# Kernel optimization log

Measured on AMD Instinct MI355X. Metric: run time of the kernel, lower is better.

Reference implementation:

```python
import jax, jax.numpy as jnp
import numpy as np

NS, NC, T, NB = 32, 16, 64, 512
NSC = NS + NC


def setup_inputs() -> dict:
    key = jax.random.key(0)
    k1, k2, k3, k4, k5 = jax.random.split(key, 5)
    # SPD cost matrices so Quu is invertible (as assumed by the LQR math)
    L = jax.random.normal(k1, (NB, T, NSC, NSC), jnp.float32) * 0.1
    Q = L @ jnp.swapaxes(L, -1, -2) + jnp.eye(NSC, dtype=jnp.float32)
    p = jax.random.normal(k2, (NB, T, NSC), jnp.float32)
    x_init = jax.random.normal(k3, (NB, NS), jnp.float32)
    # stable-ish LTI dynamics
    A = 0.9 * jnp.eye(NS, dtype=jnp.float32) + 0.01 * jax.random.normal(k4, (NS, NS), jnp.float32)
    B = 0.1 * jax.random.normal(k5, (NS, NC), jnp.float32)
    dt = jnp.float32(0.1)
    return {"x_init": x_init, "Q": Q, "p": p, "A": A, "B": B, "dt": dt}


def _lqr(x_init, Q, p, A, B):
    ns, nc = A.shape[0], B.shape[1]
    nb, Th = Q.shape[0], Q.shape[1]
    dtype = Q.dtype

    # --- nominal rollout with zero control: x_{t+1} = A x_t ---
    def roll(x, _):
        return x @ A.T, x
    _, cx = jax.lax.scan(roll, x_init, None, length=Th)   # [T,B,ns] states x_0..x_{T-1}
    cu = jnp.zeros((Th, nb, nc), dtype)                    # current_u = 0
    xu = jnp.concatenate([cx, cu], -1)                     # [T,B,nsc]

    Qs = jnp.swapaxes(Q, 0, 1)                             # [T,B,nsc,nsc]
    ps = jnp.swapaxes(p, 0, 1)                             # [T,B,nsc]
    p_new = jnp.einsum('tbij,tbj->tbi', Qs, xu) + ps       # [T,B,nsc]

    F = jnp.concatenate([A, B], axis=1)                    # [ns, nsc]

    # --- backward Riccati recursion (V=v=0 at t=T-1 makes Qt=Q[T-1]) ---
    def bwd(carry, inp):
        V, v = carry                                       # [B,ns,ns], [B,ns]
        Qt_in, qt_in = inp
        Qt = Qt_in + jnp.einsum('si,bst,tj->bij', F, V, F)
        qt = qt_in + v @ F                                 # F^T v
        Qxx, Qxu = Qt[:, :ns, :ns], Qt[:, :ns, ns:]
        Qux, Quu = Qt[:, ns:, :ns], Qt[:, ns:, ns:]
        qx, qu = qt[:, :ns], qt[:, ns:]
        Quu_inv = jnp.linalg.pinv(Quu)
        Kt = -Quu_inv @ Qux                                # [B,nc,ns]
        kt = -jnp.einsum('bij,bj->bi', Quu_inv, qu)        # [B,nc]
        KtT = jnp.swapaxes(Kt, -1, -2)
        Vn = Qxx + Qxu @ Kt + KtT @ Qux + KtT @ Quu @ Kt
        vn = (qx + jnp.einsum('bij,bj->bi', Qxu, kt)
              + jnp.einsum('bij,bj->bi', KtT, qu)
              + jnp.einsum('bij,bj->bi', KtT @ Quu, kt))
        return (Vn, vn), (Kt, kt)

    V0 = jnp.zeros((nb, ns, ns), dtype)
    v0 = jnp.zeros((nb, ns), dtype)
    _, (Ks, ks) = jax.lax.scan(bwd, (V0, v0), (Qs, p_new), reverse=True)

    # --- forward rollout with feedback policy ---
    def fwd(carry, inp):
        xt, cost = carry
        Kt, kt, cxt, cut, Qt, pt = inp
        dut = jnp.einsum('bij,bj->bi', Kt, xt - cxt) + kt
        ut = dut + cut
        xut = jnp.concatenate([xt, ut], -1)
        cost = cost + 0.5 * jnp.einsum('bi,bij,bj->b', xut, Qt, xut) + (xut * pt).sum(-1)
        xn = xt @ A.T + ut @ B.T
        return (xn, cost), (xt, ut)

    (_, cost), (xs, us) = jax.lax.scan(
        fwd, (x_init, jnp.zeros(nb, dtype)), (Ks, ks, cx, cu, Qs, ps))
    x = jnp.swapaxes(xs, 0, 1)   # [B,T,ns]  (states x_0..x_{T-1}, matching x[...,:-1,:])
    u = jnp.swapaxes(us, 0, 1)   # [B,T,nc]
    return x, u, cost


def reference(x_init, Q, p, A, B, dt):
    # dt only matters for nonlinear relinearization; with constant LTI (A,B) it is unused.
    return _lqr(x_init, Q, p, A, B)
```

## Files before the change

kernel.cpp:

```cpp
#include <hip/hip_runtime.h>


#define NSd 32
#define NCd 16
#define Td 64
#define NBd 512
#define NSCd 48

typedef __bf16 bf16x8 __attribute__((ext_vector_type(8)));
typedef __bf16 bf16x4 __attribute__((ext_vector_type(4)));
typedef float f32x4 __attribute__((ext_vector_type(4)));

#define MFMA16(a, b, c) __builtin_amdgcn_mfma_f32_16x16x32_bf16(a, b, c, 0, 0, 0)

#define XOFF ((size_t)0)
#define UOFF ((size_t)NBd * Td * NSd)
#define COFF (UOFF + (size_t)NBd * Td * NCd)

__device__ __forceinline__ float rdl(float v, int l) {
  return __uint_as_float(__builtin_amdgcn_readlane(__float_as_uint(v), l));
}

union LdsU {
  struct {
    __bf16 FTh[48][32], FTl[48][32];
    __bf16 Vh[32][32], Vl[32][32];
    __bf16 WTh[48][32], WTl[48][32];
    __bf16 Xh[32][32], Xl[32][32];
    __bf16 KTh[32][32], KTl[32][32];
    float Quu[16][17];
    float qt[48];
    float vv[32];
    float kt[16];
  } bw;
  struct {
    float K2T[2][16 * 36];
    float kv2[2][16];
    float d[32];
    float xs[32];
    float uu[16];
  } fw;
};

__global__ __launch_bounds__(256, 2) void lqr_kernel(
    const float* __restrict__ x_init, const float* __restrict__ Qg,
    const float* __restrict__ pg, const float* __restrict__ Ag,
    const float* __restrict__ Bg, float* __restrict__ out,
    float* __restrict__ wsK, float* __restrict__ wskv) {
  const int b = blockIdx.x;
  const int tid = threadIdx.x;
  const int w = tid >> 6;
  const int lane = tid & 63;
  const int fn = lane & 15;
  const int quad = lane >> 4;
  const int k0 = quad * 8;

  __shared__ __attribute__((aligned(16))) float sQ[2304];
  __shared__ float scx[Td][NSd];
  __shared__ float sFf[NSd][NSCd];
  __shared__ __attribute__((aligned(16))) LdsU U;
  __shared__ float scostp[4];

  for (int idx = tid; idx < 1536; idx += 256) {
    int i = idx / 48, j = idx - i * 48;
    sFf[i][j] = (j < 32) ? Ag[i * 32 + j] : Bg[i * 16 + (j - 32)];
  }
  for (int idx = tid; idx < 1536; idx += 256) {
    int a = idx >> 5, k = idx & 31;
    float f = (a < 32) ? Ag[k * 32 + a] : Bg[k * 16 + (a - 32)];
    __bf16 h = (__bf16)f;
    U.bw.FTh[a][k] = h;
    U.bw.FTl[a][k] = (__bf16)(f - (float)h);
  }
  for (int idx = tid; idx < 1024; idx += 256) {
    int r = idx >> 5, c = idx & 31;
    __bf16 z = (__bf16)0.f;
    U.bw.Vh[r][c] = z; U.bw.Vl[r][c] = z;
    U.bw.Xh[r][c] = z; U.bw.Xl[r][c] = z;
    U.bw.KTh[r][c] = z; U.bw.KTl[r][c] = z;
  }
  if (tid < 32) {
    scx[0][tid] = x_init[b * 32 + tid];
    U.bw.vv[tid] = 0.f;
  }
  {
    const float4* src = (const float4*)(Qg + ((size_t)b * Td + 63) * 2304);
    float4* dst = (float4*)sQ;
    dst[tid] = src[tid];
    dst[tid + 256] = src[tid + 256];
    if (tid < 64) dst[tid + 512] = src[tid + 512];
  }
  float ppf = 0.f;
  if (w == 3 && lane < 48) ppf = pg[((size_t)b * Td + 63) * 48 + lane];
  __syncthreads();

  if (w == 0) {
    for (int t2 = 0; t2 < Td - 1; ++t2) {
      if (lane < 32) {
        float acc = 0.f;
#pragma unroll
        for (int j = 0; j < 32; j += 4) {
          float4 a4 = *(const float4*)&sFf[lane][j];
          acc += a4.x * scx[t2][j] + a4.y * scx[t2][j + 1] +
                 a4.z * scx[t2][j + 2] + a4.w * scx[t2][j + 3];
        }
        scx[t2 + 1][lane] = acc;
      }
    }
  }
  __syncthreads();

  float cAcc = 0.f;
  float dAcc = 0.f;

  for (int t = Td - 1; t >= 0; --t) {
    const int sw = 3 - (t & 1);
    float4 pf0, pf1, pf2;
    float ppfn;
    if (t > 0) {
      const float4* src = (const float4*)(Qg + ((size_t)b * Td + (t - 1)) * 2304);
      pf0 = src[tid];
      pf1 = src[tid + 256];
      if (tid < 64) pf2 = src[tid + 512];
      if (w == 3 && lane < 48) ppfn = pg[((size_t)b * Td + t - 1) * 48 + lane];
    }
    if (w < 3) {
      const int I = w;
      bf16x8 aH = *(const bf16x8*)&U.bw.FTh[16 * I + fn][k0];
      bf16x8 aL = *(const bf16x8*)&U.bw.FTl[16 * I + fn][k0];
#pragma unroll
      for (int J = 0; J < 2; ++J) {
        bf16x8 bH = *(const bf16x8*)&U.bw.Vh[16 * J + fn][k0];
        bf16x8 bL = *(const bf16x8*)&U.bw.Vl[16 * J + fn][k0];
        f32x4 acc = {0.f, 0.f, 0.f, 0.f};
        acc = MFMA16(aL, bH, acc);
        acc = MFMA16(aH, bL, acc);
        acc = MFMA16(aH, bH, acc);
#pragma unroll
        for (int r = 0; r < 4; ++r) {
          float v = acc[r];
          __bf16 h = (__bf16)v;
          U.bw.WTh[16 * I + 4 * quad + r][16 * J + fn] = h;
          U.bw.WTl[16 * I + 4 * quad + r][16 * J + fn] = (__bf16)(v - (float)h);
        }
      }
    } else if (lane < 48) {
      float acc1 = ppf;
#pragma unroll
      for (int k = 0; k < 32; ++k) acc1 += sQ[k * 48 + lane] * scx[t][k];
      if (lane < 32) cAcc += 0.5f * scx[t][lane] * (acc1 + ppf);
      float acc = acc1;
#pragma unroll
      for (int k = 0; k < 32; ++k) acc += U.bw.vv[k] * sFf[k][lane];
      U.bw.qt[lane] = acc;
    }
    if (t > 0 && w == 3) ppf = ppfn;
    __syncthreads();

    f32x4 accQ = {0.f, 0.f, 0.f, 0.f};
    if (w < 2) {
      const int I = w;
      bf16x8 aH = *(const bf16x8*)&U.bw.WTh[16 * I + fn][k0];
      bf16x8 aL = *(const bf16x8*)&U.bw.WTl[16 * I + fn][k0];
      {
        bf16x8 bH = *(const bf16x8*)&U.bw.FTh[16 * I + fn][k0];
        bf16x8 bL = *(const bf16x8*)&U.bw.FTl[16 * I + fn][k0];
#pragma unroll
        for (int r = 0; r < 4; ++r)
          accQ[r] = sQ[(16 * I + 4 * quad + r) * 48 + 16 * I + fn];
        accQ = MFMA16(aL, bH, accQ);
        accQ = MFMA16(aH, bL, accQ);
        accQ = MFMA16(aH, bH, accQ);
      }
      {
        bf16x8 bH = *(const bf16x8*)&U.bw.FTh[32 + fn][k0];
        bf16x8 bL = *(const bf16x8*)&U.bw.FTl[32 + fn][k0];
        f32x4 acc;
#pragma unroll
        for (int r = 0; r < 4; ++r)
          acc[r] = sQ[(16 * I + 4 * quad + r) * 48 + 32 + fn];
        acc = MFMA16(aL, bH, acc);
        acc = MFMA16(aH, bL, acc);
        acc = MFMA16(aH, bH, acc);
#pragma unroll
        for (int r = 0; r < 4; ++r) {
          float v = acc[r];
          __bf16 h = (__bf16)v;
          U.bw.Xh[16 * I + 4 * quad + r][fn] = h;
          U.bw.Xl[16 * I + 4 * quad + r][fn] = (__bf16)(v - (float)h);
        }
      }
    } else if (w == 2) {
      bf16x8 aH = *(const bf16x8*)&U.bw.WTh[fn][k0];
      bf16x8 aL = *(const bf16x8*)&U.bw.WTl[fn][k0];
      bf16x8 bH = *(const bf16x8*)&U.bw.FTh[16 + fn][k0];
      bf16x8 bL = *(const bf16x8*)&U.bw.FTl[16 + fn][k0];
#pragma unroll
      for (int r = 0; r < 4; ++r)
        accQ[r] = sQ[(4 * quad + r) * 48 + 16 + fn];
      accQ = MFMA16(aL, bH, accQ);
      accQ = MFMA16(aH, bL, accQ);
      accQ = MFMA16(aH, bH, accQ);
    } else {
      bf16x8 aH = *(const bf16x8*)&U.bw.WTh[32 + fn][k0];
      bf16x8 aL = *(const bf16x8*)&U.bw.WTl[32 + fn][k0];
      bf16x8 bH = *(const bf16x8*)&U.bw.FTh[32 + fn][k0];
      bf16x8 bL = *(const bf16x8*)&U.bw.FTl[32 + fn][k0];
      f32x4 acc;
#pragma unroll
      for (int r = 0; r < 4; ++r)
        acc[r] = sQ[(32 + 4 * quad + r) * 48 + 32 + fn];
      acc = MFMA16(aL, bH, acc);
      acc = MFMA16(aH, bL, acc);
      acc = MFMA16(aH, bH, acc);
#pragma unroll
      for (int r = 0; r < 4; ++r) U.bw.Quu[4 * quad + r][fn] = acc[r];
    }
    __syncthreads();

    if (t > 0) {
      float4* dst = (float4*)sQ;
      dst[tid] = pf0;
      dst[tid + 256] = pf1;
      if (tid < 64) dst[tid + 512] = pf2;
    }

    if (w == sw) {
      float rhs[16];
      if (lane < 32) {
        bf16x8 xh0 = *(const bf16x8*)&U.bw.Xh[lane][0];
        bf16x8 xh1 = *(const bf16x8*)&U.bw.Xh[lane][8];
        bf16x8 xl0 = *(const bf16x8*)&U.bw.Xl[lane][0];
        bf16x8 xl1 = *(const bf16x8*)&U.bw.Xl[lane][8];
#pragma unroll
        for (int i = 0; i < 8; ++i) {
          rhs[i] = (float)xh0[i] + (float)xl0[i];
          rhs[8 + i] = (float)xh1[i] + (float)xl1[i];
        }
      } else {
#pragma unroll
        for (int i = 0; i < 16; ++i) rhs[i] = U.bw.qt[32 + i];
      }
      float quu[16];
#pragma unroll
      for (int i = 0; i < 16; ++i) quu[i] = U.bw.Quu[i][fn];
#pragma unroll
      for (int r = 0; r < 15; ++r) {
        float inv = __builtin_amdgcn_rcpf(rdl(quu[r], r));
#pragma unroll
        for (int i = r + 1; i < 16; ++i) {
          float m = rdl(quu[i], r) * inv;
          rhs[i] -= m * rhs[r];
          quu[i] -= m * quu[r];
        }
      }
      float xx[16];
#pragma unroll
      for (int r = 15; r >= 0; --r) {
        float s = rhs[r];
#pragma unroll
        for (int c = r + 1; c < 16; ++c) s -= rdl(quu[r], c) * xx[c];
        xx[r] = s * __builtin_amdgcn_rcpf(rdl(quu[r], r));
      }
      if (lane < 32) {
        bf16x8 h0, l0, h1, l1;
#pragma unroll
        for (int u = 0; u < 8; ++u) {
          float kv = -xx[u];
          __bf16 hh = (__bf16)kv;
          h0[u] = hh; l0[u] = (__bf16)(kv - (float)hh);
          float kv2 = -xx[8 + u];
          __bf16 hh2 = (__bf16)kv2;
          h1[u] = hh2; l1[u] = (__bf16)(kv2 - (float)hh2);
        }
        *(bf16x8*)&U.bw.KTh[lane][0] = h0;
        *(bf16x8*)&U.bw.KTh[lane][8] = h1;
        *(bf16x8*)&U.bw.KTl[lane][0] = l0;
        *(bf16x8*)&U.bw.KTl[lane][8] = l1;
        float4* dst = (float4*)(wsK + (((size_t)b * Td + t) * 32 + lane) * 16);
        float4 v0 = {-xx[0], -xx[1], -xx[2], -xx[3]};
        float4 v1 = {-xx[4], -xx[5], -xx[6], -xx[7]};
        float4 v2 = {-xx[8], -xx[9], -xx[10], -xx[11]};
        float4 v3 = {-xx[12], -xx[13], -xx[14], -xx[15]};
        dst[0] = v0; dst[1] = v1; dst[2] = v2; dst[3] = v3;
      } else if (lane == 32) {
#pragma unroll
        for (int u = 0; u < 16; ++u) U.bw.kt[u] = -xx[u];
        float4* dst = (float4*)(wskv + ((size_t)b * Td + t) * 16);
        float4 v0 = {-xx[0], -xx[1], -xx[2], -xx[3]};
        float4 v1 = {-xx[4], -xx[5], -xx[6], -xx[7]};
        float4 v2 = {-xx[8], -xx[9], -xx[10], -xx[11]};
        float4 v3 = {-xx[12], -xx[13], -xx[14], -xx[15]};
        dst[0] = v0; dst[1] = v1; dst[2] = v2; dst[3] = v3;
        float s = 0.f;
#pragma unroll
        for (int i = 0; i < 16; ++i) s += U.bw.qt[32 + i] * xx[i];
        dAcc -= 0.5f * s;
      }
      if (sw == 3) {
        float acc = 0.f;
        bf16x8 xh0, xh1, xl0, xl1;
        if (lane < 32) {
          xh0 = *(const bf16x8*)&U.bw.Xh[lane][0];
          xh1 = *(const bf16x8*)&U.bw.Xh[lane][8];
          xl0 = *(const bf16x8*)&U.bw.Xl[lane][0];
          xl1 = *(const bf16x8*)&U.bw.Xl[lane][8];
          acc = U.bw.qt[lane];
        }
#pragma unroll
        for (int u = 0; u < 8; ++u) {
          float kt0 = -rdl(xx[u], 32);
          float kt1 = -rdl(xx[8 + u], 32);
          if (lane < 32) {
            acc += ((float)xh0[u] + (float)xl0[u]) * kt0;
            acc += ((float)xh1[u] + (float)xl1[u]) * kt1;
          }
        }
        if (lane < 32) U.bw.vv[lane] = acc;
      }
    }
    __syncthreads();

    if (w == 0) {
      bf16x8 aH = *(const bf16x8*)&U.bw.Xh[fn][k0];
      bf16x8 aL = *(const bf16x8*)&U.bw.Xl[fn][k0];
      bf16x8 bH = *(const bf16x8*)&U.bw.KTh[fn][k0];
      bf16x8 bL = *(const bf16x8*)&U.bw.KTl[fn][k0];
      accQ = MFMA16(aL, bH, accQ);
      accQ = MFMA16(aH, bL, accQ);
      accQ = MFMA16(aH, bH, accQ);
#pragma unroll
      for (int r = 0; r < 4; ++r) {
        float v = accQ[r];
        __bf16 h = (__bf16)v;
        U.bw.Vh[4 * quad + r][fn] = h;
        U.bw.Vl[4 * quad + r][fn] = (__bf16)(v - (float)h);
      }
    } else if (w == 1) {
      bf16x8 aH = *(const bf16x8*)&U.bw.Xh[16 + fn][k0];
      bf16x8 aL = *(const bf16x8*)&U.bw.Xl[16 + fn][k0];
      bf16x8 bH = *(const bf16x8*)&U.bw.KTh[16 + fn][k0];
      bf16x8 bL = *(const bf16x8*)&U.bw.KTl[16 + fn][k0];
      accQ = MFMA16(aL, bH, accQ);
      accQ = MFMA16(aH, bL, accQ);
      accQ = MFMA16(aH, bH, accQ);
#pragma unroll
      for (int r = 0; r < 4; ++r) {
        float v = accQ[r];
        __bf16 h = (__bf16)v;
        U.bw.Vh[16 + 4 * quad + r][16 + fn] = h;
        U.bw.Vl[16 + 4 * quad + r][16 + fn] = (__bf16)(v - (float)h);
      }
    } else if (w == 2) {
      bf16x8 aH = *(const bf16x8*)&U.bw.Xh[fn][k0];
      bf16x8 aL = *(const bf16x8*)&U.bw.Xl[fn][k0];
      bf16x8 bH = *(const bf16x8*)&U.bw.KTh[16 + fn][k0];
      bf16x8 bL = *(const bf16x8*)&U.bw.KTl[16 + fn][k0];
      accQ = MFMA16(aL, bH, accQ);
      accQ = MFMA16(aH, bL, accQ);
      accQ = MFMA16(aH, bH, accQ);
      bf16x4 th, tl;
#pragma unroll
      for (int r = 0; r < 4; ++r) {
        float v = accQ[r];
        __bf16 h = (__bf16)v;
        __bf16 l = (__bf16)(v - (float)h);
        U.bw.Vh[4 * quad + r][16 + fn] = h;
        U.bw.Vl[4 * quad + r][16 + fn] = l;
        th[r] = h; tl[r] = l;
      }
      *(bf16x4*)&U.bw.Vh[16 + fn][4 * quad] = th;
      *(bf16x4*)&U.bw.Vl[16 + fn][4 * quad] = tl;
    } else if (sw == 2) {
      if (lane < 32) {
        bf16x8 xh0 = *(const bf16x8*)&U.bw.Xh[lane][0];
        bf16x8 xh1 = *(const bf16x8*)&U.bw.Xh[lane][8];
        bf16x8 xl0 = *(const bf16x8*)&U.bw.Xl[lane][0];
        bf16x8 xl1 = *(const bf16x8*)&U.bw.Xl[lane][8];
        float acc = U.bw.qt[lane];
#pragma unroll
        for (int u = 0; u < 8; ++u) {
          acc += ((float)xh0[u] + (float)xl0[u]) * U.bw.kt[u];
          acc += ((float)xh1[u] + (float)xl1[u]) * U.bw.kt[8 + u];
        }
        U.bw.vv[lane] = acc;
      }
    }
    __syncthreads();
  }

  if (w == 3) {
    float rv = (lane < 32) ? cAcc : 0.f;
    rv += __shfl_down(rv, 32);
    rv += __shfl_down(rv, 16);
    rv += __shfl_down(rv, 8);
    rv += __shfl_down(rv, 4);
    rv += __shfl_down(rv, 2);
    rv += __shfl_down(rv, 1);
    if (lane == 0) scostp[0] = rv;
  }
  if (lane == 32 && w >= 2) scostp[w - 1] = dAcc;
  __syncthreads();

  if (w == 0) {
    {
      const float4* src = (const float4*)(wsK + ((size_t)b * Td) * 512);
      float4 ka = src[lane * 2], kb = src[lane * 2 + 1];
      int jj = lane >> 1, ib = (lane & 1) * 8;
      float* kt2 = U.fw.K2T[0];
      kt2[(ib + 0) * 36 + jj] = ka.x; kt2[(ib + 1) * 36 + jj] = ka.y;
      kt2[(ib + 2) * 36 + jj] = ka.z; kt2[(ib + 3) * 36 + jj] = ka.w;
      kt2[(ib + 4) * 36 + jj] = kb.x; kt2[(ib + 5) * 36 + jj] = kb.y;
      kt2[(ib + 6) * 36 + jj] = kb.z; kt2[(ib + 7) * 36 + jj] = kb.w;
      if (lane < 16) U.fw.kv2[0][lane] = wskv[(size_t)b * Td * 16 + lane];
    }
    float xr = (lane < 32) ? scx[0][lane] : 0.f;
    for (int t = 0; t < Td; ++t) {
      const int cur = t & 1, nxt = cur ^ 1;
      float4 pa, pb;
      float pk;
      if (t < Td - 1) {
        const float4* src = (const float4*)(wsK + ((size_t)b * Td + t + 1) * 512);
        pa = src[lane * 2];
        pb = src[lane * 2 + 1];
        if (lane < 16) pk = wskv[((size_t)b * Td + t + 1) * 16 + lane];
      }
      if (lane < 32) {
        U.fw.d[lane] = xr - scx[t][lane];
        U.fw.xs[lane] = xr;
        out[XOFF + ((size_t)b * Td + t) * 32 + lane] = xr;
      }
      if (lane < 16) {
        float uv = U.fw.kv2[cur][lane];
        const float* kr = &U.fw.K2T[cur][lane * 36];
#pragma unroll
        for (int j4 = 0; j4 < 8; ++j4) {
          float4 kk = *(const float4*)&kr[j4 * 4];
          float4 dd = *(const float4*)&U.fw.d[j4 * 4];
          uv += kk.x * dd.x + kk.y * dd.y + kk.z * dd.z + kk.w * dd.w;
        }
        U.fw.uu[lane] = uv;
        out[UOFF + ((size_t)b * Td + t) * 16 + lane] = uv;
      }
      if (lane < 32) {
        float acc = 0.f;
#pragma unroll
        for (int j4 = 0; j4 < 8; ++j4) {
          float4 ff = *(const float4*)&sFf[lane][j4 * 4];
          float4 xv = *(const float4*)&U.fw.xs[j4 * 4];
          acc += ff.x * xv.x + ff.y * xv.y + ff.z * xv.z + ff.w * xv.w;
        }
#pragma unroll
        for (int j4 = 0; j4 < 4; ++j4) {
          float4 ff = *(const float4*)&sFf[lane][32 + j4 * 4];
          float4 uv = *(const float4*)&U.fw.uu[j4 * 4];
          acc += ff.x * uv.x + ff.y * uv.y + ff.z * uv.z + ff.w * uv.w;
        }
        xr = acc;
      }
      if (t < Td - 1) {
        int jj = lane >> 1, ib = (lane & 1) * 8;
        float* kt2 = U.fw.K2T[nxt];
        kt2[(ib + 0) * 36 + jj] = pa.x; kt2[(ib + 1) * 36 + jj] = pa.y;
        kt2[(ib + 2) * 36 + jj] = pa.z; kt2[(ib + 3) * 36 + jj] = pa.w;
        kt2[(ib + 4) * 36 + jj] = pb.x; kt2[(ib + 5) * 36 + jj] = pb.y;
        kt2[(ib + 6) * 36 + jj] = pb.z; kt2[(ib + 7) * 36 + jj] = pb.w;
        if (lane < 16) U.fw.kv2[nxt][lane] = pk;
      }
    }
    if (lane == 0) out[COFF + b] = scostp[0] + scostp[1] + scostp[2];
  }
}

extern "C" void kernel_launch(void* const* d_in, const int* in_sizes, int n_in,
                              void* d_out, int out_size, void* d_ws, size_t ws_size,
                              hipStream_t stream) {
  const float* x_init = (const float*)d_in[0];
  const float* Qg = (const float*)d_in[1];
  const float* pg = (const float*)d_in[2];
  const float* Ag = (const float*)d_in[3];
  const float* Bg = (const float*)d_in[4];
  float* out = (float*)d_out;
  float* wsK = (float*)d_ws;
  float* wskv = wsK + (size_t)NBd * Td * NSd * NCd;
  lqr_kernel<<<NBd, 256, 0, stream>>>(x_init, Qg, pg, Ag, Bg, out, wsK, wskv);
}
```

Baseline: 667.7 us.

## Collapse LQR block to a single wavefront, removing block barriers

Each batch block now runs as one 64-lane wavefront instead of four waves. All the Riccati MFMA work, the Quu solve and the vector updates run serially in that wave, with no __syncthreads. The union LDS layout is split into separate arrays. This removes per-step barrier latency and cross-wave handoffs, but each wave now carries all the MFMA and scalar work serially, and the Q prefetch needs 9 float4 registers per lane. In exchange, more blocks may fit per CU.

Measured after the change: 772.9 us. 1.16x slower.

```diff
diff --git a/kernel.cpp b/kernel.cpp
--- a/kernel.cpp
+++ b/kernel.cpp
@@ -5,7 +5,6 @@
 #define NCd 16
 #define Td 64
 #define NBd 512
-#define NSCd 48
 
 typedef __bf16 bf16x8 __attribute__((ext_vector_type(8)));
 typedef __bf16 bf16x4 __attribute__((ext_vector_type(4)));
@@ -21,117 +20,113 @@
   return __uint_as_float(__builtin_amdgcn_readlane(__float_as_uint(v), l));
 }
 
-union LdsU {
-  struct {
-    __bf16 FTh[48][32], FTl[48][32];
-    __bf16 Vh[32][32], Vl[32][32];
-    __bf16 WTh[48][32], WTl[48][32];
-    __bf16 Xh[32][32], Xl[32][32];
-    __bf16 KTh[32][32], KTl[32][32];
-    float Quu[16][17];
-    float qt[48];
-    float vv[32];
-    float kt[16];
-  } bw;
-  struct {
-    float K2T[2][16 * 36];
-    float kv2[2][16];
-    float d[32];
-    float xs[32];
-    float uu[16];
-  } fw;
-};
-
-__global__ __launch_bounds__(256, 2) void lqr_kernel(
+__global__ __launch_bounds__(64) void lqr_kernel(
     const float* __restrict__ x_init, const float* __restrict__ Qg,
     const float* __restrict__ pg, const float* __restrict__ Ag,
     const float* __restrict__ Bg, float* __restrict__ out,
     float* __restrict__ wsK, float* __restrict__ wskv) {
   const int b = blockIdx.x;
-  const int tid = threadIdx.x;
-  const int w = tid >> 6;
-  const int lane = tid & 63;
+  const int lane = threadIdx.x;
   const int fn = lane & 15;
   const int quad = lane >> 4;
   const int k0 = quad * 8;
 
   __shared__ __attribute__((aligned(16))) float sQ[2304];
   __shared__ float scx[Td][NSd];
-  __shared__ float sFf[NSd][NSCd];
-  __shared__ __attribute__((aligned(16))) LdsU U;
-  __shared__ float scostp[4];
-
-  for (int idx = tid; idx < 1536; idx += 256) {
+  __shared__ float sFf[NSd][48];
+  __shared__ __attribute__((aligned(16))) __bf16 FTh[48][32], FTl[48][32];
+  __shared__ __attribute__((aligned(16))) __bf16 Vh[32][32], Vl[32][32];
+  __shared__ __attribute__((aligned(16))) __bf16 WTh[48][32], WTl[48][32];
+  __shared__ __attribute__((aligned(16))) __bf16 Xh[32][32], Xl[32][32];
+  __shared__ __attribute__((aligned(16))) __bf16 KTh[32][32], KTl[32][32];
+  __shared__ float sQuu[16][17];
+  __shared__ float sqt[48];
+  __shared__ float svv[32];
+  __shared__ __attribute__((aligned(16))) float fK[2][16 * 36];
+  __shared__ float fk[2][16], fd[32], fx[32], fu[16];
+
+#pragma unroll
+  for (int ii = 0; ii < 24; ++ii) {
+    int idx = lane + 64 * ii;
     int i = idx / 48, j = idx - i * 48;
     sFf[i][j] = (j < 32) ? Ag[i * 32 + j] : Bg[i * 16 + (j - 32)];
   }
-  for (int idx = tid; idx < 1536; idx += 256) {
+#pragma unroll
+  for (int ii = 0; ii < 24; ++ii) {
+    int idx = lane + 64 * ii;
     int a = idx >> 5, k = idx & 31;
     float f = (a < 32) ? Ag[k * 32 + a] : Bg[k * 16 + (a - 32)];
     __bf16 h = (__bf16)f;
-    U.bw.FTh[a][k] = h;
-    U.bw.FTl[a][k] = (__bf16)(f - (float)h);
-  }
-  for (int idx = tid; idx < 1024; idx += 256) {
+    FTh[a][k] = h;
+    FTl[a][k] = (__bf16)(f - (float)h);
+  }
+#pragma unroll
+  for (int ii = 0; ii < 16; ++ii) {
+    int idx = lane + 64 * ii;
     int r = idx >> 5, c = idx & 31;
     __bf16 z = (__bf16)0.f;
-    U.bw.Vh[r][c] = z; U.bw.Vl[r][c] = z;
-    U.bw.Xh[r][c] = z; U.bw.Xl[r][c] = z;
-    U.bw.KTh[r][c] = z; U.bw.KTl[r][c] = z;
-  }
-  if (tid < 32) {
-    scx[0][tid] = x_init[b * 32 + tid];
-    U.bw.vv[tid] = 0.f;
+    Vh[r][c] = z; Vl[r][c] = z;
+    Xh[r][c] = z; Xl[r][c] = z;
+    KTh[r][c] = z; KTl[r][c] = z;
+  }
+  if (lane < 32) {
+    scx[0][lane] = x_init[b * 32 + lane];
+    svv[lane] = 0.f;
   }
   {
     const float4* src = (const float4*)(Qg + ((size_t)b * Td + 63) * 2304);
     float4* dst = (float4*)sQ;
-    dst[tid] = src[tid];
-    dst[tid + 256] = src[tid + 256];
-    if (tid < 64) dst[tid + 512] = src[tid + 512];
+#pragma unroll
+    for (int i = 0; i < 9; ++i) dst[lane + 64 * i] = src[lane + 64 * i];
   }
   float ppf = 0.f;
-  if (w == 3 && lane < 48) ppf = pg[((size_t)b * Td + 63) * 48 + lane];
-  __syncthreads();
-
-  if (w == 0) {
-    for (int t2 = 0; t2 < Td - 1; ++t2) {
-      if (lane < 32) {
-        float acc = 0.f;
-#pragma unroll
-        for (int j = 0; j < 32; j += 4) {
-          float4 a4 = *(const float4*)&sFf[lane][j];
-          acc += a4.x * scx[t2][j] + a4.y * scx[t2][j + 1] +
-                 a4.z * scx[t2][j + 2] + a4.w * scx[t2][j + 3];
-        }
-        scx[t2 + 1][lane] = acc;
-      }
-    }
-  }
-  __syncthreads();
+  if (lane < 48) ppf = pg[((size_t)b * Td + 63) * 48 + lane];
+
+  for (int t2 = 0; t2 < Td - 1; ++t2) {
+    if (lane < 32) {
+      float acc = 0.f;
+#pragma unroll
+      for (int j = 0; j < 32; j += 4) {
+        float4 a4 = *(const float4*)&sFf[lane][j];
+        acc += a4.x * scx[t2][j] + a4.y * scx[t2][j + 1] +
+               a4.z * scx[t2][j + 2] + a4.w * scx[t2][j + 3];
+      }
+      scx[t2 + 1][lane] = acc;
+    }
+  }
 
   float cAcc = 0.f;
   float dAcc = 0.f;
 
   for (int t = Td - 1; t >= 0; --t) {
-    const int sw = 3 - (t & 1);
-    float4 pf0, pf1, pf2;
+    float4 pf[9];
     float ppfn;
     if (t > 0) {
       const float4* src = (const float4*)(Qg + ((size_t)b * Td + (t - 1)) * 2304);
-      pf0 = src[tid];
-      pf1 = src[tid + 256];
-      if (tid < 64) pf2 = src[tid + 512];
-      if (w == 3 && lane < 48) ppfn = pg[((size_t)b * Td + t - 1) * 48 + lane];
-    }
-    if (w < 3) {
-      const int I = w;
-      bf16x8 aH = *(const bf16x8*)&U.bw.FTh[16 * I + fn][k0];
-      bf16x8 aL = *(const bf16x8*)&U.bw.FTl[16 * I + fn][k0];
+#pragma unroll
+      for (int i = 0; i < 9; ++i) pf[i] = src[lane + 64 * i];
+      if (lane < 48) ppfn = pg[((size_t)b * Td + t - 1) * 48 + lane];
+    }
+    if (lane < 48) {
+      float acc1 = ppf;
+#pragma unroll
+      for (int k = 0; k < 32; ++k) acc1 += sQ[k * 48 + lane] * scx[t][k];
+      float acc = acc1;
+#pragma unroll
+      for (int k = 0; k < 32; ++k) acc += svv[k] * sFf[k][lane];
+      sqt[lane] = acc;
+      if (lane < 32) cAcc += 0.5f * scx[t][lane] * (acc1 + ppf);
+    }
+    if (t > 0 && lane < 48) ppf = ppfn;
+
+#pragma unroll
+    for (int I = 0; I < 3; ++I) {
+      bf16x8 aH = *(const bf16x8*)&FTh[16 * I + fn][k0];
+      bf16x8 aL = *(const bf16x8*)&FTl[16 * I + fn][k0];
 #pragma unroll
       for (int J = 0; J < 2; ++J) {
-        bf16x8 bH = *(const bf16x8*)&U.bw.Vh[16 * J + fn][k0];
-        bf16x8 bL = *(const bf16x8*)&U.bw.Vl[16 * J + fn][k0];
+        bf16x8 bH = *(const bf16x8*)&Vh[16 * J + fn][k0];
+        bf16x8 bL = *(const bf16x8*)&Vl[16 * J + fn][k0];
         f32x4 acc = {0.f, 0.f, 0.f, 0.f};
         acc = MFMA16(aL, bH, acc);
         acc = MFMA16(aH, bL, acc);
@@ -140,335 +135,299 @@
         for (int r = 0; r < 4; ++r) {
           float v = acc[r];
           __bf16 h = (__bf16)v;
-          U.bw.WTh[16 * I + 4 * quad + r][16 * J + fn] = h;
-          U.bw.WTl[16 * I + 4 * quad + r][16 * J + fn] = (__bf16)(v - (float)h);
+          WTh[16 * I + 4 * quad + r][16 * J + fn] = h;
+          WTl[16 * I + 4 * quad + r][16 * J + fn] = (__bf16)(v - (float)h);
         }
       }
-    } else if (lane < 48) {
-      float acc1 = ppf;
-#pragma unroll
-      for (int k = 0; k < 32; ++k) acc1 += sQ[k * 48 + lane] * scx[t][k];
-      if (lane < 32) cAcc += 0.5f * scx[t][lane] * (acc1 + ppf);
-      float acc = acc1;
-#pragma unroll
-      for (int k = 0; k < 32; ++k) acc += U.bw.vv[k] * sFf[k][lane];
-      U.bw.qt[lane] = acc;
-    }
-    if (t > 0 && w == 3) ppf = ppfn;
-    __syncthreads();
-
-    f32x4 accQ = {0.f, 0.f, 0.f, 0.f};
-    if (w < 2) {
-      const int I = w;
-      bf16x8 aH = *(const bf16x8*)&U.bw.WTh[16 * I + fn][k0];
-      bf16x8 aL = *(const bf16x8*)&U.bw.WTl[16 * I + fn][k0];
-      {
-        bf16x8 bH = *(const bf16x8*)&U.bw.FTh[16 * I + fn][k0];
-        bf16x8 bL = *(const bf16x8*)&U.bw.FTl[16 * I + fn][k0];
-#pragma unroll
-        for (int r = 0; r < 4; ++r)
-          accQ[r] = sQ[(16 * I + 4 * quad + r) * 48 + 16 * I + fn];
-        accQ = MFMA16(aL, bH, accQ);
-        accQ = MFMA16(aH, bL, accQ);
-        accQ = MFMA16(aH, bH, accQ);
-      }
-      {
-        bf16x8 bH = *(const bf16x8*)&U.bw.FTh[32 + fn][k0];
-        bf16x8 bL = *(const bf16x8*)&U.bw.FTl[32 + fn][k0];
-        f32x4 acc;
-#pragma unroll
-        for (int r = 0; r < 4; ++r)
-          acc[r] = sQ[(16 * I + 4 * quad + r) * 48 + 32 + fn];
-        acc = MFMA16(aL, bH, acc);
-        acc = MFMA16(aH, bL, acc);
-        acc = MFMA16(aH, bH, acc);
-#pragma unroll
-        for (int r = 0; r < 4; ++r) {
-          float v = acc[r];
-          __bf16 h = (__bf16)v;
-          U.bw.Xh[16 * I + 4 * quad + r][fn] = h;
-          U.bw.Xl[16 * I + 4 * quad + r][fn] = (__bf16)(v - (float)h);
-        }
-      }
-    } else if (w == 2) {
-      bf16x8 aH = *(const bf16x8*)&U.bw.WTh[fn][k0];
-      bf16x8 aL = *(const bf16x8*)&U.bw.WTl[fn][k0];
-      bf16x8 bH = *(const bf16x8*)&U.bw.FTh[16 + fn][k0];
-      bf16x8 bL = *(const bf16x8*)&U.bw.FTl[16 + fn][k0];
-#pragma unroll
-      for (int r = 0; r < 4; ++r)
-        accQ[r] = sQ[(4 * quad + r) * 48 + 16 + fn];
-      accQ = MFMA16(aL, bH, accQ);
-      accQ = MFMA16(aH, bL, accQ);
-      accQ = MFMA16(aH, bH, accQ);
-    } else {
-      bf16x8 aH = *(const bf16x8*)&U.bw.WTh[32 + fn][k0];
-      bf16x8 aL = *(const bf16x8*)&U.bw.WTl[32 + fn][k0];
-      bf16x8 bH = *(const bf16x8*)&U.bw.FTh[32 + fn][k0];
-      bf16x8 bL = *(const bf16x8*)&U.bw.FTl[32 + fn][k0];
+    }
+
+    bf16x8 wt0H = *(const bf16x8*)&WTh[fn][k0];
+    bf16x8 wt0L = *(const bf16x8*)&WTl[fn][k0];
+    bf16x8 wt1H = *(const bf16x8*)&WTh[16 + fn][k0];
+    bf16x8 wt1L = *(const bf16x8*)&WTl[16 + fn][k0];
+    bf16x8 wt2H = *(const bf16x8*)&WTh[32 + fn][k0];
+    bf16x8 wt2L = *(const bf16x8*)&WTl[32 + fn][k0];
+    bf16x8 ft0H = *(const bf16x8*)&FTh[fn][k0];
+    bf16x8 ft0L = *(const bf16x8*)&FTl[fn][k0];
+    bf16x8 ft1H = *(const bf16x8*)&FTh[16 + fn][k0];
+    bf16x8 ft1L = *(const bf16x8*)&FTl[16 + fn][k0];
+    bf16x8 ft2H = *(const bf16x8*)&FTh[32 + fn][k0];
+    bf16x8 ft2L = *(const bf16x8*)&FTl[32 + fn][k0];
+    f32x4 accQ0, accQ1, accQ2;
+#pragma unroll
+    for (int r = 0; r < 4; ++r) {
+      accQ0[r] = sQ[(4 * quad + r) * 48 + fn];
+      accQ1[r] = sQ[(16 + 4 * quad + r) * 48 + 16 + fn];
+      accQ2[r] = sQ[(4 * quad + r) * 48 + 16 + fn];
+    }
+    accQ0 = MFMA16(wt0L, ft0H, accQ0);
+    accQ0 = MFMA16(wt0H, ft0L, accQ0);
+    accQ0 = MFMA16(wt0H, ft0H, accQ0);
+    accQ1 = MFMA16(wt1L, ft1H, accQ1);
+    accQ1 = MFMA16(wt1H, ft1L, accQ1);
+    accQ1 = MFMA16(wt1H, ft1H, accQ1);
+    accQ2 = MFMA16(wt0L, ft1H, accQ2);
+    accQ2 = MFMA16(wt0H, ft1L, accQ2);
+    accQ2 = MFMA16(wt0H, ft1H, accQ2);
+    {
       f32x4 acc;
 #pragma unroll
-      for (int r = 0; r < 4; ++r)
-        acc[r] = sQ[(32 + 4 * quad + r) * 48 + 32 + fn];
-      acc = MFMA16(aL, bH, acc);
-      acc = MFMA16(aH, bL, acc);
-      acc = MFMA16(aH, bH, acc);
-#pragma unroll
-      for (int r = 0; r < 4; ++r) U.bw.Quu[4 * quad + r][fn] = acc[r];
-    }
-    __syncthreads();
-
+      for (int r = 0; r < 4; ++r) acc[r] = sQ[(4 * quad + r) * 48 + 32 + fn];
+      acc = MFMA16(wt0L, ft2H, acc);
+      acc = MFMA16(wt0H, ft2L, acc);
+      acc = MFMA16(wt0H, ft2H, acc);
+#pragma unroll
+      for (int r = 0; r < 4; ++r) {
+        float v = acc[r];
+        __bf16 h = (__bf16)v;
+        Xh[4 * quad + r][fn] = h;
+        Xl[4 * quad + r][fn] = (__bf16)(v - (float)h);
+      }
+    }
+    {
+      f32x4 acc;
+#pragma unroll
+      for (int r = 0; r < 4; ++r) acc[r] = sQ[(16 + 4 * quad + r) * 48 + 32 + fn];
+      acc = MFMA16(wt1L, ft2H, acc);
+      acc = MFMA16(wt1H, ft2L, acc);
+      acc = MFMA16(wt1H, ft2H, acc);
+#pragma unroll
+      for (int r = 0; r < 4; ++r) {
+        float v = acc[r];
+        __bf16 h = (__bf16)v;
+        Xh[16 + 4 * quad + r][fn] = h;
+        Xl[16 + 4 * quad + r][fn] = (__bf16)(v - (float)h);
+      }
+    }
+    {
+      f32x4 acc;
+#pragma unroll
+      for (int r = 0; r < 4; ++r) acc[r] = sQ[(32 + 4 * quad + r) * 48 + 32 + fn];
+      acc = MFMA16(wt2L, ft2H, acc);
+      acc = MFMA16(wt2H, ft2L, acc);
+      acc = MFMA16(wt2H, ft2H, acc);
+#pragma unroll
+      for (int r = 0; r < 4; ++r) sQuu[4 * quad + r][fn] = acc[r];
+    }
     if (t > 0) {
       float4* dst = (float4*)sQ;
-      dst[tid] = pf0;
-      dst[tid + 256] = pf1;
-      if (tid < 64) dst[tid + 512] = pf2;
-    }
-
-    if (w == sw) {
-      float rhs[16];
-      if (lane < 32) {
-        bf16x8 xh0 = *(const bf16x8*)&U.bw.Xh[lane][0];
-        bf16x8 xh1 = *(const bf16x8*)&U.bw.Xh[lane][8];
-        bf16x8 xl0 = *(const bf16x8*)&U.bw.Xl[lane][0];
-        bf16x8 xl1 = *(const bf16x8*)&U.bw.Xl[lane][8];
-#pragma unroll
-        for (int i = 0; i < 8; ++i) {
-          rhs[i] = (float)xh0[i] + (float)xl0[i];
-          rhs[8 + i] = (float)xh1[i] + (float)xl1[i];
-        }
-      } else {
-#pragma unroll
-        for (int i = 0; i < 16; ++i) rhs[i] = U.bw.qt[32 + i];
-      }
-      float quu[16];
-#pragma unroll
-      for (int i = 0; i < 16; ++i) quu[i] = U.bw.Quu[i][fn];
-#pragma unroll
-      for (int r = 0; r < 15; ++r) {
-        float inv = __builtin_amdgcn_rcpf(rdl(quu[r], r));
-#pragma unroll
-        for (int i = r + 1; i < 16; ++i) {
-          float m = rdl(quu[i], r) * inv;
-          rhs[i] -= m * rhs[r];
-          quu[i] -= m * quu[r];
-        }
-      }
-      float xx[16];
-#pragma unroll
-      for (int r = 15; r >= 0; --r) {
-        float s = rhs[r];
-#pragma unroll
-        for (int c = r + 1; c < 16; ++c) s -= rdl(quu[r], c) * xx[c];
-        xx[r] = s * __builtin_amdgcn_rcpf(rdl(quu[r], r));
-      }
-      if (lane < 32) {
-        bf16x8 h0, l0, h1, l1;
-#pragma unroll
-        for (int u = 0; u < 8; ++u) {
-          float kv = -xx[u];
-          __bf16 hh = (__bf16)kv;
-          h0[u] = hh; l0[u] = (__bf16)(kv - (float)hh);
-          float kv2 = -xx[8 + u];
-          __bf16 hh2 = (__bf16)kv2;
-          h1[u] = hh2; l1[u] = (__bf16)(kv2 - (float)hh2);
-        }
-        *(bf16x8*)&U.bw.KTh[lane][0] = h0;
-        *(bf16x8*)&U.bw.KTh[lane][8] = h1;
-        *(bf16x8*)&U.bw.KTl[lane][0] = l0;
-        *(bf16x8*)&U.bw.KTl[lane][8] = l1;
-        float4* dst = (float4*)(wsK + (((size_t)b * Td + t) * 32 + lane) * 16);
-        float4 v0 = {-xx[0], -xx[1], -xx[2], -xx[3]};
-        float4 v1 = {-xx[4], -xx[5], -xx[6], -xx[7]};
-        float4 v2 = {-xx[8], -xx[9], -xx[10], -xx[11]};
-        float4 v3 = {-xx[12], -xx[13], -xx[14], -xx[15]};
-        dst[0] = v0; dst[1] = v1; dst[2] = v2; dst[3] = v3;
-      } else if (lane == 32) {
-#pragma unroll
-        for (int u = 0; u < 16; ++u) U.bw.kt[u] = -xx[u];
-        float4* dst = (float4*)(wskv + ((size_t)b * Td + t) * 16);
-        float4 v0 = {-xx[0], -xx[1], -xx[2], -xx[3]};
-        float4 v1 = {-xx[4], -xx[5], -xx[6], -xx[7]};
-        float4 v2 = {-xx[8], -xx[9], -xx[10], -xx[11]};
-        float4 v3 = {-xx[12], -xx[13], -xx[14], -xx[15]};
-        dst[0] = v0; dst[1] = v1; dst[2] = v2; dst[3] = v3;
-        float s = 0.f;
-#pragma unroll
-        for (int i = 0; i < 16; ++i) s += U.bw.qt[32 + i] * xx[i];
-        dAcc -= 0.5f * s;
-      }
-      if (sw == 3) {
-        float acc = 0.f;
-        bf16x8 xh0, xh1, xl0, xl1;
-        if (lane < 32) {
-          xh0 = *(const bf16x8*)&U.bw.Xh[lane][0];
-          xh1 = *(const bf16x8*)&U.bw.Xh[lane][8];
-          xl0 = *(const bf16x8*)&U.bw.Xl[lane][0];
-          xl1 = *(const bf16x8*)&U.bw.Xl[lane][8];
-          acc = U.bw.qt[lane];
-        }
-#pragma unroll
-        for (int u = 0; u < 8; ++u) {
-          float kt0 = -rdl(xx[u], 32);
-          float kt1 = -rdl(xx[8 + u], 32);
-          if (lane < 32) {
-            acc += ((float)xh0[u] + (float)xl0[u]) * kt0;
-            acc += ((float)xh1[u] + (float)xl1[u]) * kt1;
-          }
-        }
-        if (lane < 32) U.bw.vv[lane] = acc;
-      }
-    }
-    __syncthreads();
-
-    if (w == 0) {
-      bf16x8 aH = *(const bf16x8*)&U.bw.Xh[fn][k0];
-      bf16x8 aL = *(const bf16x8*)&U.bw.Xl[fn][k0];
-      bf16x8 bH = *(const bf16x8*)&U.bw.KTh[fn][k0];
-      bf16x8 bL = *(const bf16x8*)&U.bw.KTl[fn][k0];
-      accQ = MFMA16(aL, bH, accQ);
-      accQ = MFMA16(aH, bL, accQ);
-      accQ = MFMA16(aH, bH, accQ);
+#pragma unroll
+      for (int i = 0; i < 9; ++i) dst[lane + 64 * i] = pf[i];
+    }
+
+    float rhs[16];
+    if (lane < 32) {
+      bf16x8 xh0 = *(const bf16x8*)&Xh[lane][0];
+      bf16x8 xh1 = *(const bf16x8*)&Xh[lane][8];
+      bf16x8 xl0 = *(const bf16x8*)&Xl[lane][0];
+      bf16x8 xl1 = *(const bf16x8*)&Xl[lane][8];
+#pragma unroll
+      for (int i = 0; i < 8; ++i) {
+        rhs[i] = (float)xh0[i] + (float)xl0[i];
+        rhs[8 + i] = (float)xh1[i] + (float)xl1[i];
+      }
+    } else {
+#pragma unroll
+      for (int i = 0; i < 16; ++i) rhs[i] = sqt[32 + i];
+    }
+    float quu[16];
+#pragma unroll
+    for (int i = 0; i < 16; ++i) quu[i] = sQuu[i][fn];
+#pragma unroll
+    for (int r = 0; r < 15; ++r) {
+      float inv = __builtin_amdgcn_rcpf(rdl(quu[r], r));
+#pragma unroll
+      for (int i = r + 1; i < 16; ++i) {
+        float m = rdl(quu[i], r) * inv;
+        rhs[i] -= m * rhs[r];
+        quu[i] -= m * quu[r];
+      }
+    }
+    float xx[16];
+#pragma unroll
+    for (int r = 15; r >= 0; --r) {
+      float xr = rhs[r] * __builtin_amdgcn_rcpf(rdl(quu[r], r));
+      xx[r] = xr;
+#pragma unroll
+      for (int i = 0; i < r; ++i) rhs[i] -= rdl(quu[i], r) * xr;
+    }
+    if (lane < 32) {
+      bf16x8 h0, l0, h1, l1;
+#pragma unroll
+      for (int u = 0; u < 8; ++u) {
+        float kv = -xx[u];
+        __bf16 hh = (__bf16)kv;
+        h0[u] = hh; l0[u] = (__bf16)(kv - (float)hh);
+        float kv2 = -xx[8 + u];
+        __bf16 hh2 = (__bf16)kv2;
+        h1[u] = hh2; l1[u] = (__bf16)(kv2 - (float)hh2);
+      }
+      *(bf16x8*)&KTh[lane][0] = h0;
+      *(bf16x8*)&KTh[lane][8] = h1;
+      *(bf16x8*)&KTl[lane][0] = l0;
+      *(bf16x8*)&KTl[lane][8] = l1;
+      float4* dst = (float4*)(wsK + (((size_t)b * Td + t) * 32 + lane) * 16);
+      float4 v0 = {-xx[0], -xx[1], -xx[2], -xx[3]};
+      float4 v1 = {-xx[4], -xx[5], -xx[6], -xx[7]};
+      float4 v2 = {-xx[8], -xx[9], -xx[10], -xx[11]};
+      float4 v3 = {-xx[12], -xx[13], -xx[14], -xx[15]};
+      dst[0] = v0; dst[1] = v1; dst[2] = v2; dst[3] = v3;
+    } else if (lane == 32) {
+      float4* dst = (float4*)(wskv + ((size_t)b * Td + t) * 16);
+      float4 v0 = {-xx[0], -xx[1], -xx[2], -xx[3]};
+      float4 v1 = {-xx[4], -xx[5], -xx[6], -xx[7]};
+      float4 v2 = {-xx[8], -xx[9], -xx[10], -xx[11]};
+      float4 v3 = {-xx[12], -xx[13], -xx[14], -xx[15]};
+      dst[0] = v0; dst[1] = v1; dst[2] = v2; dst[3] = v3;
+      float s = 0.f;
+#pragma unroll
+      for (int i = 0; i < 16; ++i) s += sqt[32 + i] * xx[i];
+      dAcc -= 0.5f * s;
+    }
+
+    {
+      bf16x8 x0H = *(const bf16x8*)&Xh[fn][k0];
+      bf16x8 x0L = *(const bf16x8*)&Xl[fn][k0];
+      bf16x8 x1H = *(const bf16x8*)&Xh[16 + fn][k0];
+      bf16x8 x1L = *(const bf16x8*)&Xl[16 + fn][k0];
+      bf16x8 kt0H = *(const bf16x8*)&KTh[fn][k0];
+      bf16x8 kt0L = *(const bf16x8*)&KTl[fn][k0];
+      bf16x8 kt1H = *(const bf16x8*)&KTh[16 + fn][k0];
+      bf16x8 kt1L = *(const bf16x8*)&KTl[16 + fn][k0];
+      accQ0 = MFMA16(x0L, kt0H, accQ0);
+      accQ0 = MFMA16(x0H, kt0L, accQ0);
+      accQ0 = MFMA16(x0H, kt0H, accQ0);
+      accQ1 = MFMA16(x1L, kt1H, accQ1);
+      accQ1 = MFMA16(x1H, kt1L, accQ1);
+      accQ1 = MFMA16(x1H, kt1H, accQ1);
+      accQ2 = MFMA16(x0L, kt1H, accQ2);
+      accQ2 = MFMA16(x0H, kt1L, accQ2);
+      accQ2 = MFMA16(x0H, kt1H, accQ2);
 #pragma unroll
       for (int r = 0; r < 4; ++r) {
-        float v = accQ[r];
+        float v = accQ0[r];
         __bf16 h = (__bf16)v;
-        U.bw.Vh[4 * quad + r][fn] = h;
-        U.bw.Vl[4 * quad + r][fn] = (__bf16)(v - (float)h);
-      }
-    } else if (w == 1) {
-      bf16x8 aH = *(const bf16x8*)&U.bw.Xh[16 + fn][k0];
-      bf16x8 aL = *(const bf16x8*)&U.bw.Xl[16 + fn][k0];
-      bf16x8 bH = *(const bf16x8*)&U.bw.KTh[16 + fn][k0];
-      bf16x8 bL = *(const bf16x8*)&U.bw.KTl[16 + fn][k0];
-      accQ = MFMA16(aL, bH, accQ);
-      accQ = MFMA16(aH, bL, accQ);
-      accQ = MFMA16(aH, bH, accQ);
+        Vh[4 * quad + r][fn] = h;
+        Vl[4 * quad + r][fn] = (__bf16)(v - (float)h);
+      }
 #pragma unroll
       for (int r = 0; r < 4; ++r) {
-        float v = accQ[r];
+        float v = accQ1[r];
         __bf16 h = (__bf16)v;
-        U.bw.Vh[16 + 4 * quad + r][16 + fn] = h;
-        U.bw.Vl[16 + 4 * quad + r][16 + fn] = (__bf16)(v - (float)h);
-      }
-    } else if (w == 2) {
-      bf16x8 aH = *(const bf16x8*)&U.bw.Xh[fn][k0];
-      bf16x8 aL = *(const bf16x8*)&U.bw.Xl[fn][k0];
-      bf16x8 bH = *(const bf16x8*)&U.bw.KTh[16 + fn][k0];
-      bf16x8 bL = *(const bf16x8*)&U.bw.KTl[16 + fn][k0];
-      accQ = MFMA16(aL, bH, accQ);
-      accQ = MFMA16(aH, bL, accQ);
-      accQ = MFMA16(aH, bH, accQ);
+        Vh[16 + 4 * quad + r][16 + fn] = h;
+        Vl[16 + 4 * quad + r][16 + fn] = (__bf16)(v - (float)h);
+      }
       bf16x4 th, tl;
 #pragma unroll
       for (int r = 0; r < 4; ++r) {
-        float v = accQ[r];
+        float v = accQ2[r];
         __bf16 h = (__bf16)v;
         __bf16 l = (__bf16)(v - (float)h);
-        U.bw.Vh[4 * quad + r][16 + fn] = h;
-        U.bw.Vl[4 * quad + r][16 + fn] = l;
+        Vh[4 * quad + r][16 + fn] = h;
+        Vl[4 * quad + r][16 + fn] = l;
         th[r] = h; tl[r] = l;
       }
-      *(bf16x4*)&U.bw.Vh[16 + fn][4 * quad] = th;
-      *(bf16x4*)&U.bw.Vl[16 + fn][4 * quad] = tl;
-    } else if (sw == 2) {
+      *(bf16x4*)&Vh[16 + fn][4 * quad] = th;
+      *(bf16x4*)&Vl[16 + fn][4 * quad] = tl;
+    }
+    {
+      float acc = 0.f;
+      bf16x8 xh0, xh1, xl0, xl1;
       if (lane < 32) {
-        bf16x8 xh0 = *(const bf16x8*)&U.bw.Xh[lane][0];
-        bf16x8 xh1 = *(const bf16x8*)&U.bw.Xh[lane][8];
-        bf16x8 xl0 = *(const bf16x8*)&U.bw.Xl[lane][0];
-        bf16x8 xl1 = *(const bf16x8*)&U.bw.Xl[lane][8];
-        float acc = U.bw.qt[lane];
-#pragma unroll
-        for (int u = 0; u < 8; ++u) {
-          acc += ((float)xh0[u] + (float)xl0[u]) * U.bw.kt[u];
-          acc += ((float)xh1[u] + (float)xl1[u]) * U.bw.kt[8 + u];
+        xh0 = *(const bf16x8*)&Xh[lane][0];
+        xh1 = *(const bf16x8*)&Xh[lane][8];
+        xl0 = *(const bf16x8*)&Xl[lane][0];
+        xl1 = *(const bf16x8*)&Xl[lane][8];
+        acc = sqt[lane];
+      }
+#pragma unroll
+      for (int u = 0; u < 8; ++u) {
+        float kt0 = -rdl(xx[u], 32);
+        float kt1 = -rdl(xx[8 + u], 32);
+        if (lane < 32) {
+          acc += ((float)xh0[u] + (float)xl0[u]) * kt0;
+          acc += ((float)xh1[u] + (float)xl1[u]) * kt1;
         }
-        U.bw.vv[lane] = acc;
-      }
-    }
-    __syncthreads();
-  }
-
-  if (w == 3) {
-    float rv = (lane < 32) ? cAcc : 0.f;
+      }
+      if (lane < 32) svv[lane] = acc;
+    }
+  }
+
+  {
+    float rv = (lane < 32) ? cAcc : ((lane == 32) ? dAcc : 0.f);
     rv += __shfl_down(rv, 32);
     rv += __shfl_down(rv, 16);
     rv += __shfl_down(rv, 8);
     rv += __shfl_down(rv, 4);
     rv += __shfl_down(rv, 2);
     rv += __shfl_down(rv, 1);
-    if (lane == 0) scostp[0] = rv;
-  }
-  if (lane == 32 && w >= 2) scostp[w - 1] = dAcc;
-  __syncthreads();
-
-  if (w == 0) {
-    {
-      const float4* src = (const float4*)(wsK + ((size_t)b * Td) * 512);
-      float4 ka = src[lane * 2], kb = src[lane * 2 + 1];
+    if (lane == 0) out[COFF + b] = rv;
+  }
+
+  {
+    const float4* src = (const float4*)(wsK + ((size_t)b * Td) * 512);
+    float4 ka = src[lane * 2], kb = src[lane * 2 + 1];
+    int jj = lane >> 1, ib = (lane & 1) * 8;
+    float* kt2 = fK[0];
+    kt2[(ib + 0) * 36 + jj] = ka.x; kt2[(ib + 1) * 36 + jj] = ka.y;
+    kt2[(ib + 2) * 36 + jj] = ka.z; kt2[(ib + 3) * 36 + jj] = ka.w;
+    kt2[(ib + 4) * 36 + jj] = kb.x; kt2[(ib + 5) * 36 + jj] = kb.y;
+    kt2[(ib + 6) * 36 + jj] = kb.z; kt2[(ib + 7) * 36 + jj] = kb.w;
+    if (lane < 16) fk[0][lane] = wskv[(size_t)b * Td * 16 + lane];
+  }
+  float xr = (lane < 32) ? scx[0][lane] : 0.f;
+  for (int t = 0; t < Td; ++t) {
+    const int cur = t & 1, nxt = cur ^ 1;
+    float4 pa, pb;
+    float pk;
+    if (t < Td - 1) {
+      const float4* src = (const float4*)(wsK + ((size_t)b * Td + t + 1) * 512);
+      pa = src[lane * 2];
+      pb = src[lane * 2 + 1];
+      if (lane < 16) pk = wskv[((size_t)b * Td + t + 1) * 16 + lane];
+    }
+    if (lane < 32) {
+      fd[lane] = xr - scx[t][lane];
+      fx[lane] = xr;
+      out[XOFF + ((size_t)b * Td + t) * 32 + lane] = xr;
+    }
+    if (lane < 16) {
+      float uv = fk[cur][lane];
+      const float* kr = &fK[cur][lane * 36];
+#pragma unroll
+      for (int j4 = 0; j4 < 8; ++j4) {
+        float4 kk = *(const float4*)&kr[j4 * 4];
+        float4 dd = *(const float4*)&fd[j4 * 4];
+        uv += kk.x * dd.x + kk.y * dd.y + kk.z * dd.z + kk.w * dd.w;
+      }
+      fu[lane] = uv;
+      out[UOFF + ((size_t)b * Td + t) * 16 + lane] = uv;
+    }
+    if (lane < 32) {
+      float acc = 0.f;
+#pragma unroll
+      for (int j4 = 0; j4 < 8; ++j4) {
+        float4 ff = *(const float4*)&sFf[lane][j4 * 4];
+        float4 xv = *(const float4*)&fx[j4 * 4];
+        acc += ff.x * xv.x + ff.y * xv.y + ff.z * xv.z + ff.w * xv.w;
+      }
+#pragma unroll
+      for (int j4 = 0; j4 < 4; ++j4) {
+        float4 ff = *(const float4*)&sFf[lane][32 + j4 * 4];
+        float4 uv = *(const float4*)&fu[j4 * 4];
+        acc += ff.x * uv.x + ff.y * uv.y + ff.z * uv.z + ff.w * uv.w;
+      }
+      xr = acc;
+    }
+    if (t < Td - 1) {
       int jj = lane >> 1, ib = (lane & 1) * 8;
-      float* kt2 = U.fw.K2T[0];
-      kt2[(ib + 0) * 36 + jj] = ka.x; kt2[(ib + 1) * 36 + jj] = ka.y;
-      kt2[(ib + 2) * 36 + jj] = ka.z; kt2[(ib + 3) * 36 + jj] = ka.w;
-      kt2[(ib + 4) * 36 + jj] = kb.x; kt2[(ib + 5) * 36 + jj] = kb.y;
-      kt2[(ib + 6) * 36 + jj] = kb.z; kt2[(ib + 7) * 36 + jj] = kb.w;
-      if (lane < 16) U.fw.kv2[0][lane] = wskv[(size_t)b * Td * 16 + lane];
-    }
-    float xr = (lane < 32) ? scx[0][lane] : 0.f;
-    for (int t = 0; t < Td; ++t) {
-      const int cur = t & 1, nxt = cur ^ 1;
-      float4 pa, pb;
-      float pk;
-      if (t < Td - 1) {
-        const float4* src = (const float4*)(wsK + ((size_t)b * Td + t + 1) * 512);
-        pa = src[lane * 2];
-        pb = src[lane * 2 + 1];
-        if (lane < 16) pk = wskv[((size_t)b * Td + t + 1) * 16 + lane];
-      }
-      if (lane < 32) {
-        U.fw.d[lane] = xr - scx[t][lane];
-        U.fw.xs[lane] = xr;
-        out[XOFF + ((size_t)b * Td + t) * 32 + lane] = xr;
-      }
-      if (lane < 16) {
-        float uv = U.fw.kv2[cur][lane];
-        const float* kr = &U.fw.K2T[cur][lane * 36];
-#pragma unroll
-        for (int j4 = 0; j4 < 8; ++j4) {
-          float4 kk = *(const float4*)&kr[j4 * 4];
-          float4 dd = *(const float4*)&U.fw.d[j4 * 4];
-          uv += kk.x * dd.x + kk.y * dd.y + kk.z * dd.z + kk.w * dd.w;
-        }
-        U.fw.uu[lane] = uv;
-        out[UOFF + ((size_t)b * Td + t) * 16 + lane] = uv;
-      }
-      if (lane < 32) {
-        float acc = 0.f;
-#pragma unroll
-        for (int j4 = 0; j4 < 8; ++j4) {
-          float4 ff = *(const float4*)&sFf[lane][j4 * 4];
-          float4 xv = *(const float4*)&U.fw.xs[j4 * 4];
-          acc += ff.x * xv.x + ff.y * xv.y + ff.z * xv.z + ff.w * xv.w;
-        }
-#pragma unroll
-        for (int j4 = 0; j4 < 4; ++j4) {
-          float4 ff = *(const float4*)&sFf[lane][32 + j4 * 4];
-          float4 uv = *(const float4*)&U.fw.uu[j4 * 4];
-          acc += ff.x * uv.x + ff.y * uv.y + ff.z * uv.z + ff.w * uv.w;
-        }
-        xr = acc;
-      }
-      if (t < Td - 1) {
-        int jj = lane >> 1, ib = (lane & 1) * 8;
-        float* kt2 = U.fw.K2T[nxt];
-        kt2[(ib + 0) * 36 + jj] = pa.x; kt2[(ib + 1) * 36 + jj] = pa.y;
-        kt2[(ib + 2) * 36 + jj] = pa.z; kt2[(ib + 3) * 36 + jj] = pa.w;
-        kt2[(ib + 4) * 36 + jj] = pb.x; kt2[(ib + 5) * 36 + jj] = pb.y;
-        kt2[(ib + 6) * 36 + jj] = pb.z; kt2[(ib + 7) * 36 + jj] = pb.w;
-        if (lane < 16) U.fw.kv2[nxt][lane] = pk;
-      }
-    }
-    if (lane == 0) out[COFF + b] = scostp[0] + scostp[1] + scostp[2];
+      float* kt2 = fK[nxt];
+      kt2[(ib + 0) * 36 + jj] = pa.x; kt2[(ib + 1) * 36 + jj] = pa.y;
+      kt2[(ib + 2) * 36 + jj] = pa.z; kt2[(ib + 3) * 36 + jj] = pa.w;
+      kt2[(ib + 4) * 36 + jj] = pb.x; kt2[(ib + 5) * 36 + jj] = pb.y;
+      kt2[(ib + 6) * 36 + jj] = pb.z; kt2[(ib + 7) * 36 + jj] = pb.w;
+      if (lane < 16) fk[nxt][lane] = pk;
+    }
   }
 }
 
@@ -483,5 +442,5 @@
   float* out = (float*)d_out;
   float* wsK = (float*)d_ws;
   float* wskv = wsK + (size_t)NBd * Td * NSd * NCd;
-  lqr_kernel<<<NBd, 256, 0, stream>>>(x_init, Qg, pg, Ag, Bg, out, wsK, wskv);
+  lqr_kernel<<<NBd, 64, 0, stream>>>(x_init, Qg, pg, Ag, Bg, out, wsK, wskv);
 }
```
